# Optimization experiments

Hardware: AMD Instinct MI355X
Metric: run time of the kernel (lower is better)

## Reference

```python
import jax, jax.numpy as jnp
import numpy as np

N, F, H, D = 4096, 128, 8, 8  # nodes, in_feat, head_num, att_embedding_size
EDGE_PROB = 0.01
NEG_INF = -1e10  # original uses -10e9 * (1 - A)


def setup_inputs() -> dict:
    key = jax.random.key(0)
    k1, k2, k3, k4, k5 = jax.random.split(key, 5)
    X = jax.random.normal(k1, (N, F), dtype=jnp.float32)
    # binary dense adjacency with self-loops (faithful to the dense-mask GAT formulation)
    A = (jax.random.uniform(k2, (N, N)) < EDGE_PROB).astype(jnp.float32)
    A = jnp.maximum(A, jnp.eye(N, dtype=jnp.float32))
    W = jax.random.normal(k3, (F, H * D), dtype=jnp.float32) * 0.05
    att_self = jax.random.normal(k4, (1, H, D), dtype=jnp.float32) * 0.05
    att_neigh = jax.random.normal(k5, (1, H, D), dtype=jnp.float32) * 0.05
    bias = jnp.zeros((1, H, D), dtype=jnp.float32)
    return {"X": X, "A": A, "W": W, "att_self": att_self,
            "att_neigh": att_neigh, "bias": bias}


def reference(X, A, W, att_self, att_neigh, bias):
    # per-head linear projection: [N, H, D]
    feats = (X @ W).reshape(N, H, D)
    # attention scores a_self^T h_i and a_neigh^T h_j : [N, H]
    a_s = jnp.sum(feats * att_self, axis=-1)
    a_n = jnp.sum(feats * att_neigh, axis=-1)
    # dense logits [H, N, N]: logits[h,i,j] = a_s[i,h] + a_n[j,h]
    logits = a_s.T[:, :, None] + a_n.T[:, None, :]
    logits = jax.nn.leaky_relu(logits, 0.2)
    logits = logits + NEG_INF * (1.0 - A)[None, :, :]
    attn = jax.nn.softmax(logits, axis=-1)  # [H, N, N]
    # weighted neighbor aggregation: [N, H, D]
    out = jnp.einsum('hij,jhd->ihd', attn, feats)
    out = out + bias  # use_bias=True
    out = out.reshape(N, H * D)  # reduction='concat'
    return jax.nn.relu(out)  # activation=relu
```

## Files before the change

kernel.cpp:

```cpp
#include <hip/hip_runtime.h>
#include <hip/hip_bf16.h>

#define NNODES 4096
#define FIN    128
#define NH     8
#define HD     8
#define HDOUT  64
#define MAXNZ  512
#define NPB    4

typedef __hip_bfloat16 bf16;

template<typename T>
__device__ __forceinline__ float ld1(const void* p, int idx) {
    if constexpr (sizeof(T) == 2) return __bfloat162float(((const bf16*)p)[idx]);
    else                          return ((const float*)p)[idx];
}
template<typename T>
__device__ __forceinline__ void st1(void* p, int idx, float v) {
    if constexpr (sizeof(T) == 2) ((bf16*)p)[idx] = __float2bfloat16(v);
    else                          ((float*)p)[idx] = v;
}

__device__ __forceinline__ bool a_is_bf16(const void* A) {
    return ((*(const unsigned*)A) & 0xFFFFu) == 0x3F80u;
}

template<typename T>
__device__ __forceinline__ void proj_body(
    const void* A, const void* X, const void* W,
    const void* att_s, const void* att_n,
    float* feats, float* a_s, float* a_n, int* nz_cnt, int* nz_idx,
    int i0, int w, int t, float (*xs)[FIN])
{
    const int tid = (w << 6) | t;

    xs[tid >> 7][tid & 127]       = ld1<T>(X, (i0 +     (tid >> 7)) * FIN + (tid & 127));
    xs[2 + (tid >> 7)][tid & 127] = ld1<T>(X, (i0 + 2 + (tid >> 7)) * FIN + (tid & 127));
    __syncthreads();

    const int i = i0 + w;

    {
        const float* x = xs[w];
        float acc = 0.f;
        #pragma unroll 16
        for (int f = 0; f < FIN; ++f)
            acc += x[f] * ld1<T>(W, f * HDOUT + t);

        feats[(size_t)i * HDOUT + t] = acc;

        float vs = acc * ld1<T>(att_s, t);
        float vn = acc * ld1<T>(att_n, t);
        #pragma unroll
        for (int m = 1; m < 8; m <<= 1) {
            vs += __shfl_xor(vs, m, 8);
            vn += __shfl_xor(vn, m, 8);
        }
        if ((t & 7) == 0) {
            a_s[i * NH + (t >> 3)] = vs;
            a_n[i * NH + (t >> 3)] = vn;
        }
    }

    unsigned long long m = 0ull;
    if constexpr (sizeof(T) == 2) {
        const ushort4* row = (const ushort4*)((const bf16*)A + (size_t)i * NNODES);
        #pragma unroll
        for (int it = 0; it < 16; ++it) {
            ushort4 v = row[it * 64 + t];
            unsigned nib = (v.x != 0) | ((v.y != 0) << 1) | ((v.z != 0) << 2) | ((v.w != 0) << 3);
            m |= (unsigned long long)nib << (it * 4);
        }
    } else {
        const uint4* row = (const uint4*)((const float*)A + (size_t)i * NNODES);
        #pragma unroll
        for (int it = 0; it < 16; ++it) {
            uint4 v = row[it * 64 + t];
            unsigned nib = (v.x != 0) | ((v.y != 0) << 1) | ((v.z != 0) << 2) | ((v.w != 0) << 3);
            m |= (unsigned long long)nib << (it * 4);
        }
    }
    int cnt = __popcll(m);

    int inc = cnt;
    #pragma unroll
    for (int d = 1; d < 64; d <<= 1) {
        int o = __shfl_up(inc, d, 64);
        if (t >= d) inc += o;
    }
    int off   = inc - cnt;
    int total = __shfl(inc, 63, 64);
    if (t == 0) nz_cnt[i] = (total < MAXNZ) ? total : MAXNZ;

    int* dst = nz_idx + (size_t)i * MAXNZ;
    while (m) {
        int b = __ffsll((long long)m) - 1;
        m &= m - 1;
        if (off < MAXNZ)
            dst[off++] = ((b >> 2) << 8) + (t << 2) + (b & 3);
    }
}

__global__ __launch_bounds__(256) void k_proj(
    const void* __restrict__ A, const void* __restrict__ X, const void* __restrict__ W,
    const void* __restrict__ att_s, const void* __restrict__ att_n,
    float* __restrict__ feats, float* __restrict__ a_s, float* __restrict__ a_n,
    int* __restrict__ nz_cnt, int* __restrict__ nz_idx)
{
    __shared__ float xs[NPB][FIN];
    const int w = threadIdx.x >> 6, t = threadIdx.x & 63;
    const int i0 = blockIdx.x * NPB;
    if (a_is_bf16(A)) proj_body<bf16 >(A, X, W, att_s, att_n, feats, a_s, a_n, nz_cnt, nz_idx, i0, w, t, xs);
    else              proj_body<float>(A, X, W, att_s, att_n, feats, a_s, a_n, nz_cnt, nz_idx, i0, w, t, xs);
}

template<typename T>
__device__ __forceinline__ void gat_body(
    const int* nz_cnt, const int* nz_idx, const float* feats,
    const float* a_s, const float* a_n, const void* bias, void* out,
    int i, int tid, int* s_idx, float (*s_num)[HDOUT], float (*s_den)[HDOUT])
{
    const int K = nz_cnt[i];
    for (int k = tid; k < K; k += 256)
        s_idx[k] = nz_idx[(size_t)i * MAXNZ + k];
    __syncthreads();

    const int rep = tid >> 6;
    const int u   = tid & 63;
    const int h   = u >> 3;
    const float ash = a_s[i * NH + h];

    float num = 0.f, den = 0.f;
    int k = rep;
    #pragma unroll 2
    for (; k + 4 < K; k += 8) {
        int ja = s_idx[k];
        int jb = s_idx[k + 4];
        float ana = a_n[ja * NH + h];
        float anb = a_n[jb * NH + h];
        float fa  = feats[(size_t)ja * HDOUT + u];
        float fb  = feats[(size_t)jb * HDOUT + u];
        float za = ash + ana; za = (za >= 0.f) ? za : 0.2f * za;
        float zb = ash + anb; zb = (zb >= 0.f) ? zb : 0.2f * zb;
        float ea = __expf(za);
        float eb = __expf(zb);
        num += ea * fa + eb * fb;
        den += ea + eb;
    }
    if (k < K) {
        int j = s_idx[k];
        float z = ash + a_n[j * NH + h];
        z = (z >= 0.f) ? z : 0.2f * z;
        float e = __expf(z);
        num += e * feats[(size_t)j * HDOUT + u];
        den += e;
    }
    s_num[rep][u] = num;
    s_den[rep][u] = den;
    __syncthreads();

    if (tid < HDOUT) {
        float n = s_num[0][u] + s_num[1][u] + s_num[2][u] + s_num[3][u];
        float d = s_den[0][u] + s_den[1][u] + s_den[2][u] + s_den[3][u];
        float v = n / d + ld1<T>(bias, u);
        st1<T>(out, i * HDOUT + u, fmaxf(v, 0.f));
    }
}

__global__ __launch_bounds__(256) void k_gat(
    const void* __restrict__ A,
    const int* __restrict__ nz_cnt, const int* __restrict__ nz_idx,
    const float* __restrict__ feats, const float* __restrict__ a_s,
    const float* __restrict__ a_n, const void* __restrict__ bias,
    void* __restrict__ out)
{
    __shared__ int   s_idx[MAXNZ];
    __shared__ float s_num[4][HDOUT];
    __shared__ float s_den[4][HDOUT];
    const int i = blockIdx.x, tid = threadIdx.x;
    if (a_is_bf16(A)) gat_body<bf16 >(nz_cnt, nz_idx, feats, a_s, a_n, bias, out, i, tid, s_idx, s_num, s_den);
    else              gat_body<float>(nz_cnt, nz_idx, feats, a_s, a_n, bias, out, i, tid, s_idx, s_num, s_den);
}

extern "C" void kernel_launch(void* const* d_in, const int* in_sizes, int n_in,
                              void* d_out, int out_size, void* d_ws, size_t ws_size,
                              hipStream_t stream) {
    const void* X     = d_in[0];
    const void* A     = d_in[1];
    const void* W     = d_in[2];
    const void* att_s = d_in[3];
    const void* att_n = d_in[4];
    const void* bias  = d_in[5];

    float* feats  = (float*)d_ws;
    float* as_    = feats + (size_t)NNODES * HDOUT;
    float* an_    = as_   + (size_t)NNODES * NH;
    int*   nz_cnt = (int*)(an_ + (size_t)NNODES * NH);
    int*   nz_idx = nz_cnt + NNODES;

    hipLaunchKernelGGL(k_proj, dim3(NNODES / NPB), dim3(256), 0, stream,
                       A, X, W, att_s, att_n, feats, as_, an_, nz_cnt, nz_idx);
    hipLaunchKernelGGL(k_gat,  dim3(NNODES), dim3(256), 0, stream,
                       A, nz_cnt, nz_idx, feats, as_, an_, bias, d_out);
}
```

Baseline: 113.0 us.

## Use one wavefront per node in GAT aggregation and remap projection threads

The aggregation kernel now gives each output node a single 64-lane wavefront instead of a 256-thread block. Each wave reads neighbor indices straight from global memory and unrolls by four with predicated tails, which removes the shared-memory staging, both block barriers and the cross-wave reduction. The grid shrinks to NNODES/4 blocks. The projection kernel remaps threads so each wave computes 16 output columns for all four nodes, and pads the shared X tile to 132 floats. The trade-off is less parallelism per node on the serial neighbor loop (~40 neighbors), which lengthens each wave's latency chain.

```diff
diff --git a/kernel.cpp b/kernel.cpp
--- a/kernel.cpp
+++ b/kernel.cpp
@@ -8,6 +8,7 @@
 #define HDOUT  64
 #define MAXNZ  512
 #define NPB    4
+#define XSP    132
 
 typedef __hip_bfloat16 bf16;
 
@@ -31,38 +32,43 @@
     const void* A, const void* X, const void* W,
     const void* att_s, const void* att_n,
     float* feats, float* a_s, float* a_n, int* nz_cnt, int* nz_idx,
-    int i0, int w, int t, float (*xs)[FIN])
+    int i0, int w, int t, float (*xs)[XSP])
 {
     const int tid = (w << 6) | t;
 
-    xs[tid >> 7][tid & 127]       = ld1<T>(X, (i0 +     (tid >> 7)) * FIN + (tid & 127));
-    xs[2 + (tid >> 7)][tid & 127] = ld1<T>(X, (i0 + 2 + (tid >> 7)) * FIN + (tid & 127));
+    {
+        const int r = tid >> 7, c = tid & 127;
+        xs[r][c]     = ld1<T>(X, (i0 + r)     * FIN + c);
+        xs[r + 2][c] = ld1<T>(X, (i0 + r + 2) * FIN + c);
+    }
     __syncthreads();
 
-    const int i = i0 + w;
-
     {
-        const float* x = xs[w];
+        const int n = t >> 4;
+        const int c = (w << 4) | (t & 15);
+        const float* x = xs[n];
         float acc = 0.f;
         #pragma unroll 16
         for (int f = 0; f < FIN; ++f)
-            acc += x[f] * ld1<T>(W, f * HDOUT + t);
+            acc += x[f] * ld1<T>(W, f * HDOUT + c);
 
-        feats[(size_t)i * HDOUT + t] = acc;
+        feats[(size_t)(i0 + n) * HDOUT + c] = acc;
 
-        float vs = acc * ld1<T>(att_s, t);
-        float vn = acc * ld1<T>(att_n, t);
+        float vs = acc * ld1<T>(att_s, c);
+        float vn = acc * ld1<T>(att_n, c);
         #pragma unroll
         for (int m = 1; m < 8; m <<= 1) {
             vs += __shfl_xor(vs, m, 8);
             vn += __shfl_xor(vn, m, 8);
         }
         if ((t & 7) == 0) {
-            a_s[i * NH + (t >> 3)] = vs;
-            a_n[i * NH + (t >> 3)] = vn;
+            const int h = c >> 3;
+            a_s[(i0 + n) * NH + h] = vs;
+            a_n[(i0 + n) * NH + h] = vn;
         }
     }
 
+    const int i = i0 + w;
     unsigned long long m = 0ull;
     if constexpr (sizeof(T) == 2) {
         const ushort4* row = (const ushort4*)((const bf16*)A + (size_t)i * NNODES);
@@ -108,7 +114,7 @@
     float* __restrict__ feats, float* __restrict__ a_s, float* __restrict__ a_n,
     int* __restrict__ nz_cnt, int* __restrict__ nz_idx)
 {
-    __shared__ float xs[NPB][FIN];
+    __shared__ float xs[NPB][XSP];
     const int w = threadIdx.x >> 6, t = threadIdx.x & 63;
     const int i0 = blockIdx.x * NPB;
     if (a_is_bf16(A)) proj_body<bf16 >(A, X, W, att_s, att_n, feats, a_s, a_n, nz_cnt, nz_idx, i0, w, t, xs);
@@ -119,53 +125,42 @@
 __device__ __forceinline__ void gat_body(
     const int* nz_cnt, const int* nz_idx, const float* feats,
     const float* a_s, const float* a_n, const void* bias, void* out,
-    int i, int tid, int* s_idx, float (*s_num)[HDOUT], float (*s_den)[HDOUT])
+    int i, int t)
 {
     const int K = nz_cnt[i];
-    for (int k = tid; k < K; k += 256)
-        s_idx[k] = nz_idx[(size_t)i * MAXNZ + k];
-    __syncthreads();
-
-    const int rep = tid >> 6;
-    const int u   = tid & 63;
-    const int h   = u >> 3;
+    const int h = t >> 3;
     const float ash = a_s[i * NH + h];
+    const int* idx = nz_idx + (size_t)i * MAXNZ;
 
     float num = 0.f, den = 0.f;
-    int k = rep;
-    #pragma unroll 2
-    for (; k + 4 < K; k += 8) {
-        int ja = s_idx[k];
-        int jb = s_idx[k + 4];
-        float ana = a_n[ja * NH + h];
-        float anb = a_n[jb * NH + h];
-        float fa  = feats[(size_t)ja * HDOUT + u];
-        float fb  = feats[(size_t)jb * HDOUT + u];
-        float za = ash + ana; za = (za >= 0.f) ? za : 0.2f * za;
-        float zb = ash + anb; zb = (zb >= 0.f) ? zb : 0.2f * zb;
-        float ea = __expf(za);
-        float eb = __expf(zb);
-        num += ea * fa + eb * fb;
-        den += ea + eb;
+    for (int k = 0; k < K; k += 4) {
+        const bool v1 = (k + 1 < K), v2 = (k + 2 < K), v3 = (k + 3 < K);
+        const int j0 = idx[k];
+        const int j1 = idx[v1 ? k + 1 : k];
+        const int j2 = idx[v2 ? k + 2 : k];
+        const int j3 = idx[v3 ? k + 3 : k];
+        const float an0 = a_n[j0 * NH + h];
+        const float an1 = a_n[j1 * NH + h];
+        const float an2 = a_n[j2 * NH + h];
+        const float an3 = a_n[j3 * NH + h];
+        const float f0 = feats[(size_t)j0 * HDOUT + t];
+        const float f1 = feats[(size_t)j1 * HDOUT + t];
+        const float f2 = feats[(size_t)j2 * HDOUT + t];
+        const float f3 = feats[(size_t)j3 * HDOUT + t];
+        float z0 = ash + an0; z0 = (z0 >= 0.f) ? z0 : 0.2f * z0;
+        float z1 = ash + an1; z1 = (z1 >= 0.f) ? z1 : 0.2f * z1;
+        float z2 = ash + an2; z2 = (z2 >= 0.f) ? z2 : 0.2f * z2;
+        float z3 = ash + an3; z3 = (z3 >= 0.f) ? z3 : 0.2f * z3;
+        const float e0 = __expf(z0);
+        const float e1 = v1 ? __expf(z1) : 0.f;
+        const float e2 = v2 ? __expf(z2) : 0.f;
+        const float e3 = v3 ? __expf(z3) : 0.f;
+        num += e0 * f0 + e1 * f1 + e2 * f2 + e3 * f3;
+        den += e0 + e1 + e2 + e3;
     }
-    if (k < K) {
-        int j = s_idx[k];
-        float z = ash + a_n[j * NH + h];
-        z = (z >= 0.f) ? z : 0.2f * z;
-        float e = __expf(z);
-        num += e * feats[(size_t)j * HDOUT + u];
-        den += e;
-    }
-    s_num[rep][u] = num;
-    s_den[rep][u] = den;
-    __syncthreads();
 
-    if (tid < HDOUT) {
-        float n = s_num[0][u] + s_num[1][u] + s_num[2][u] + s_num[3][u];
-        float d = s_den[0][u] + s_den[1][u] + s_den[2][u] + s_den[3][u];
-        float v = n / d + ld1<T>(bias, u);
-        st1<T>(out, i * HDOUT + u, fmaxf(v, 0.f));
-    }
+    const float r = num / den + ld1<T>(bias, t);
+    st1<T>(out, i * HDOUT + t, fmaxf(r, 0.f));
 }
 
 __global__ __launch_bounds__(256) void k_gat(
@@ -175,12 +170,10 @@
     const float* __restrict__ a_n, const void* __restrict__ bias,
     void* __restrict__ out)
 {
-    __shared__ int   s_idx[MAXNZ];
-    __shared__ float s_num[4][HDOUT];
-    __shared__ float s_den[4][HDOUT];
-    const int i = blockIdx.x, tid = threadIdx.x;
-    if (a_is_bf16(A)) gat_body<bf16 >(nz_cnt, nz_idx, feats, a_s, a_n, bias, out, i, tid, s_idx, s_num, s_den);
-    else              gat_body<float>(nz_cnt, nz_idx, feats, a_s, a_n, bias, out, i, tid, s_idx, s_num, s_den);
+    const int i = blockIdx.x * NPB + (threadIdx.x >> 6);
+    const int t = threadIdx.x & 63;
+    if (a_is_bf16(A)) gat_body<bf16 >(nz_cnt, nz_idx, feats, a_s, a_n, bias, out, i, t);
+    else              gat_body<float>(nz_cnt, nz_idx, feats, a_s, a_n, bias, out, i, t);
 }
 
 extern "C" void kernel_launch(void* const* d_in, const int* in_sizes, int n_in,
@@ -201,6 +194,6 @@
 
     hipLaunchKernelGGL(k_proj, dim3(NNODES / NPB), dim3(256), 0, stream,
                        A, X, W, att_s, att_n, feats, as_, an_, nz_cnt, nz_idx);
-    hipLaunchKernelGGL(k_gat,  dim3(NNODES), dim3(256), 0, stream,
+    hipLaunchKernelGGL(k_gat,  dim3(NNODES / NPB), dim3(256), 0, stream,
                        A, nz_cnt, nz_idx, feats, as_, an_, bias, d_out);
 }
```

Result: slower. 117.3 us (+3.8%).
